# Optimization experiments

Measured on AMD Instinct MI355X. Metric: run time of the kernel, lower is better.

Reference implementation:

```python
import jax, jax.numpy as jnp
import numpy as np

B, S, D = 8, 4096, 1024
MINR, MAXR = 0.9, 0.999


def setup_inputs() -> dict:
    key = jax.random.key(0)
    ks = jax.random.split(key, 10)

    def dense(k, fin, fout):
        # lecun_normal-style init for flax nn.Dense kernels
        return jax.random.normal(k, (fin, fout), jnp.float32) * (fin ** -0.5)

    x = jax.random.normal(ks[0], (B, S, D), jnp.float32)
    # RNN 'a' param: stable_init -> uniform in [min_rad, max_rad]
    a_fwd = jax.random.uniform(ks[1], (D,), jnp.float32, MINR, MAXR)
    # RGLRU 'a' param: recurrence_init
    u = jax.random.uniform(ks[2], (D,), jnp.float32)
    log_rad = 0.5 * jnp.log(u * (MAXR ** 2 - MINR ** 2) + MINR ** 2)
    a_param = jnp.log(jnp.exp(-log_rad) - 1.0)
    return {
        "x": x,
        "a_fwd": a_fwd,
        "Wf1": dense(ks[3], D, D), "bf1": jnp.zeros((D,), jnp.float32),
        "Wf2": dense(ks[4], D, D), "bf2": jnp.zeros((D,), jnp.float32),
        "Wbx": dense(ks[5], D, D), "bbx": jnp.zeros((D,), jnp.float32),
        "Wgx": dense(ks[6], D, D), "bgx": jnp.zeros((D,), jnp.float32),
        "Wga": dense(ks[7], D, D), "bga": jnp.zeros((D,), jnp.float32),
        "a_param": a_param,
        "Wb2": dense(ks[8], D, D), "bb2": jnp.zeros((D,), jnp.float32),
    }


def reference(x, a_fwd, Wf1, bf1, Wf2, bf2, Wbx, bbx, Wgx, bgx, Wga, bga,
              a_param, Wb2, bb2):
    b = x.shape[0]
    d = Wf1.shape[1]
    identity = x
    xg = jax.nn.gelu(x)  # flax nn.gelu default = tanh approximation

    # ---- forward branch: plain linear RNN  h = a*h + x_t ----
    u = xg @ Wf1 + bf1                       # [B,S,D]
    u_sf = jnp.swapaxes(u, 0, 1)             # [S,B,D]

    def step_f(h, ut):
        h = a_fwd * h + ut
        return h, h

    _, hf = jax.lax.scan(step_f, jnp.zeros((b, d), u.dtype), u_sf)
    out_f = jnp.swapaxes(hf, 0, 1) @ Wf2 + bf2

    # ---- backward branch: RG-LRU, reversed scan ----
    v = xg @ Wbx + bbx                       # [B,S,D]
    gate_x = jax.nn.sigmoid(v @ Wgx + bgx)
    gate_a = jax.nn.sigmoid(v @ Wga + bga)
    log_a = -8.0 * gate_a * jax.nn.softplus(a_param)
    a = jnp.exp(log_a)                       # [B,S,D]
    # h = a*h + sqrt(1 - a^2) * (gate_x * v)
    scaled_in = jnp.sqrt(1.0 - jnp.exp(2.0 * log_a)) * (gate_x * v)

    a_sf = jnp.swapaxes(a, 0, 1)             # [S,B,D]
    in_sf = jnp.swapaxes(scaled_in, 0, 1)    # [S,B,D]

    def step_b(h, inp):
        a_t, g_t = inp
        h = a_t * h + g_t
        return h, h

    _, hb = jax.lax.scan(step_b, jnp.zeros((b, d), v.dtype), (a_sf, in_sf),
                         reverse=True)
    out_b = jnp.swapaxes(hb, 0, 1) @ Wb2 + bb2

    return out_f + out_b + identity
```

## Files before the change

### kernel.cpp

```cpp
#include <hip/hip_runtime.h>

typedef __bf16 bf16;
typedef __bf16 bf16x8 __attribute__((ext_vector_type(8)));
typedef float floatx4 __attribute__((ext_vector_type(4)));

typedef __attribute__((address_space(1))) const void gvoid_t;
typedef __attribute__((address_space(3))) void lvoid_t;

#define B_DIM 8
#define S_DIM 4096
#define M_DIM 32768
#define CHUNK 128
#define NCHUNK 32

__device__ __forceinline__ void gload_lds16(const bf16* g, bf16* l) {
    __builtin_amdgcn_global_load_lds((gvoid_t*)g, (lvoid_t*)l, 16, 0, 0);
}

__device__ __forceinline__ float gelu_tanh(float x) {
    float x3 = x * x * x;
    return 0.5f * x * (1.0f + tanhf(0.7978845608028654f * (x + 0.044715f * x3)));
}

__device__ __forceinline__ float sigmoidf(float z) {
    return 1.0f / (1.0f + expf(-z));
}

__global__ void prep_weights(const float* __restrict__ W0, const float* __restrict__ W1,
                             const float* __restrict__ W2, const float* __restrict__ W3,
                             const float* __restrict__ W4, const float* __restrict__ W5,
                             bf16* __restrict__ T0, bf16* __restrict__ T1,
                             bf16* __restrict__ T2, bf16* __restrict__ T3,
                             bf16* __restrict__ T4, bf16* __restrict__ T5) {
    __shared__ float tile[32][33];
    int mz = blockIdx.z;
    const float* W = mz == 0 ? W0 : mz == 1 ? W1 : mz == 2 ? W2 : mz == 3 ? W3 : mz == 4 ? W4 : W5;
    bf16* T = mz == 0 ? T0 : mz == 1 ? T1 : mz == 2 ? T2 : mz == 3 ? T3 : mz == 4 ? T4 : T5;
    int tn = blockIdx.x * 32;
    int tk = blockIdx.y * 32;
    int tx = threadIdx.x & 31, ty = threadIdx.x >> 5;
#pragma unroll
    for (int i = 0; i < 4; ++i)
        tile[ty + i * 8][tx] = W[(size_t)(tk + ty + i * 8) * 1024 + tn + tx];
    __syncthreads();
#pragma unroll
    for (int i = 0; i < 4; ++i)
        T[(size_t)(tn + ty + i * 8) * 1024 + tk + tx] = (bf16)tile[tx][ty + i * 8];
}

__global__ void sp_kernel(const float* __restrict__ a_param, float* __restrict__ spbuf) {
    int d = blockIdx.x * 256 + threadIdx.x;
    spbuf[d] = log1pf(expf(a_param[d]));
}

__global__ void gelu_kernel(const float* __restrict__ x, bf16* __restrict__ xg) {
    size_t i = (size_t)blockIdx.x * 256 + threadIdx.x;
    float4 v = ((const float4*)x)[i];
    bf16 o0 = (bf16)gelu_tanh(v.x), o1 = (bf16)gelu_tanh(v.y);
    bf16 o2 = (bf16)gelu_tanh(v.z), o3 = (bf16)gelu_tanh(v.w);
    typedef __bf16 bf16x4 __attribute__((ext_vector_type(4)));
    bf16x4 o = {o0, o1, o2, o3};
    ((bf16x4*)xg)[i] = o;
}

template <int MODE>
__launch_bounds__(256, 2)
__global__ void gemm_k1024(const bf16* __restrict__ A, const bf16* __restrict__ Bt,
                           float* __restrict__ outf, bf16* __restrict__ outh,
                           const float* __restrict__ bias,
                           const float* __restrict__ auxf,
                           const bf16* __restrict__ labuf,
                           const bf16* __restrict__ vbuf,
                           const float* __restrict__ bias2) {
    __shared__ __align__(16) bf16 lsA[128 * 64];
    __shared__ __align__(16) bf16 lsB[128 * 64];
    const int tid = threadIdx.x;
    const int wave = tid >> 6;
    const int lane = tid & 63;
    const int lane15 = lane & 15;
    const int quad = lane >> 4;
    const int wm = wave & 1, wn = wave >> 1;
    const int blk = blockIdx.x;
    const int xcd = blk & 7;
    const int j = blk >> 3;
    const long m0 = (long)(xcd * 32 + (j >> 3)) * 128;
    const long n0 = (long)(j & 7) * 128;
    const int r_in = lane >> 3;
    const int cch = lane & 7;

    floatx4 acc[4][4] = {};

    for (int kt = 0; kt < 16; ++kt) {
        __syncthreads();
#pragma unroll
        for (int i = 0; i < 4; ++i) {
            int rr = (i * 4 + wave) * 8 + r_in;
            int g = cch ^ (rr & 7);
            gload_lds16(A + (size_t)(m0 + rr) * 1024 + kt * 64 + g * 8, &lsA[(i * 4 + wave) * 512]);
            gload_lds16(Bt + (size_t)(n0 + rr) * 1024 + kt * 64 + g * 8, &lsB[(i * 4 + wave) * 512]);
        }
        __syncthreads();
#pragma unroll
        for (int kk = 0; kk < 2; ++kk) {
            bf16x8 af[4], bfr[4];
#pragma unroll
            for (int mi = 0; mi < 4; ++mi) {
                int ml = wm * 64 + mi * 16 + lane15;
                af[mi] = *(const bf16x8*)&lsA[ml * 64 + ((kk * 4 + quad) ^ (ml & 7)) * 8];
            }
#pragma unroll
            for (int ni = 0; ni < 4; ++ni) {
                int nl = wn * 64 + ni * 16 + lane15;
                bfr[ni] = *(const bf16x8*)&lsB[nl * 64 + ((kk * 4 + quad) ^ (nl & 7)) * 8];
            }
#pragma unroll
            for (int mi = 0; mi < 4; ++mi)
#pragma unroll
                for (int ni = 0; ni < 4; ++ni)
                    acc[mi][ni] = __builtin_amdgcn_mfma_f32_16x16x32_bf16(af[mi], bfr[ni], acc[mi][ni], 0, 0, 0);
        }
    }

#pragma unroll
    for (int mi = 0; mi < 4; ++mi) {
#pragma unroll
        for (int ni = 0; ni < 4; ++ni) {
            floatx4 v = acc[mi][ni];
            long gn = n0 + wn * 64 + ni * 16 + lane15;
#pragma unroll
            for (int r = 0; r < 4; ++r) {
                long gm = m0 + wm * 64 + mi * 16 + quad * 4 + r;
                size_t o = (size_t)gm * 1024 + gn;
                if (MODE == 0) {
                    outf[o] = v[r] + bias[gn];
                } else if (MODE == 1) {
                    outh[o] = (bf16)(v[r] + bias[gn]);
                } else if (MODE == 2) {
                    float z = v[r] + bias[gn];
                    outh[o] = (bf16)(-8.0f * sigmoidf(z) * auxf[gn]);
                } else if (MODE == 3) {
                    float z = v[r] + bias[gn];
                    float laf = (float)labuf[o];
                    float sc = sqrtf(-expm1f(2.0f * laf)) * sigmoidf(z) * (float)vbuf[o];
                    outh[o] = (bf16)sc;
                } else if (MODE == 4) {
                    outf[o] = v[r] + bias[gn] + bias2[gn] + auxf[o];
                } else {
                    outf[o] += v[r];
                }
            }
        }
    }
}

__global__ void fscan1(const float* __restrict__ u, const float* __restrict__ a_fwd,
                       float* __restrict__ carry) {
    int d = (blockIdx.x & 3) * 256 + threadIdx.x;
    int c = (blockIdx.x >> 2) & 31;
    int b = blockIdx.x >> 7;
    float a = a_fwd[d];
    const float* up = u + ((size_t)(b * S_DIM + c * CHUNK)) * 1024 + d;
    float h = 0.0f;
#pragma unroll 8
    for (int t = 0; t < CHUNK; ++t) h = fmaf(a, h, up[(size_t)t * 1024]);
    carry[((size_t)c * 8 + b) * 1024 + d] = h;
}
__global__ void fscan2(const float* __restrict__ carry, const float* __restrict__ a_fwd,
                       float* __restrict__ H) {
    int idx = blockIdx.x * 256 + threadIdx.x;
    int d = idx & 1023, b = idx >> 10;
    float a = a_fwd[d];
    float aL = a;
#pragma unroll
    for (int i = 0; i < 7; ++i) aL *= aL;
    float h = 0.0f;
    for (int c = 0; c < NCHUNK; ++c) {
        size_t o = ((size_t)c * 8 + b) * 1024 + d;
        H[o] = h;
        h = fmaf(aL, h, carry[o]);
    }
}
__global__ void fscan3(const float* __restrict__ u, const float* __restrict__ a_fwd,
                       const float* __restrict__ H, bf16* __restrict__ hf) {
    int d = (blockIdx.x & 3) * 256 + threadIdx.x;
    int c = (blockIdx.x >> 2) & 31;
    int b = blockIdx.x >> 7;
    float a = a_fwd[d];
    const float* up = u + ((size_t)(b * S_DIM + c * CHUNK)) * 1024 + d;
    bf16* op = hf + ((size_t)(b * S_DIM + c * CHUNK)) * 1024 + d;
    float h = H[((size_t)c * 8 + b) * 1024 + d];
#pragma unroll 4
    for (int t = 0; t < CHUNK; ++t) {
        h = fmaf(a, h, up[(size_t)t * 1024]);
        op[(size_t)t * 1024] = (bf16)h;
    }
}

__global__ void bscan1(const bf16* __restrict__ la, const bf16* __restrict__ sc,
                       float* __restrict__ BL, float* __restrict__ BP) {
    int d = (blockIdx.x & 3) * 256 + threadIdx.x;
    int c = (blockIdx.x >> 2) & 31;
    int b = blockIdx.x >> 7;
    const bf16* lap = la + ((size_t)(b * S_DIM + c * CHUNK)) * 1024 + d;
    const bf16* gp = sc + ((size_t)(b * S_DIM + c * CHUNK)) * 1024 + d;
    float h = 0.0f, slog = 0.0f;
#pragma unroll 4
    for (int t = CHUNK - 1; t >= 0; --t) {
        float laf = (float)lap[(size_t)t * 1024];
        h = fmaf(expf(laf), h, (float)gp[(size_t)t * 1024]);
        slog += laf;
    }
    size_t o = ((size_t)c * 8 + b) * 1024 + d;
    BL[o] = h;
    BP[o] = expf(slog);
}
__global__ void bscan2(const float* __restrict__ BL, const float* __restrict__ BP,
                       float* __restrict__ R) {
    int idx = blockIdx.x * 256 + threadIdx.x;
    int d = idx & 1023, b = idx >> 10;
    float r = 0.0f;
    for (int c = NCHUNK - 1; c >= 0; --c) {
        size_t o = ((size_t)c * 8 + b) * 1024 + d;
        R[o] = r;
        r = fmaf(BP[o], r, BL[o]);
    }
}
__global__ void bscan3(const bf16* __restrict__ la, const bf16* __restrict__ sc,
                       const float* __restrict__ R, bf16* __restrict__ hb) {
    int d = (blockIdx.x & 3) * 256 + threadIdx.x;
    int c = (blockIdx.x >> 2) & 31;
    int b = blockIdx.x >> 7;
    const bf16* lap = la + ((size_t)(b * S_DIM + c * CHUNK)) * 1024 + d;
    const bf16* gp = sc + ((size_t)(b * S_DIM + c * CHUNK)) * 1024 + d;
    bf16* op = hb + ((size_t)(b * S_DIM + c * CHUNK)) * 1024 + d;
    float h = R[((size_t)c * 8 + b) * 1024 + d];
#pragma unroll 4
    for (int t = CHUNK - 1; t >= 0; --t) {
        h = fmaf(expf((float)lap[(size_t)t * 1024]), h, (float)gp[(size_t)t * 1024]);
        op[(size_t)t * 1024] = (bf16)h;
    }
}

extern "C" void kernel_launch(void* const* d_in, const int* in_sizes, int n_in,
                              void* d_out, int out_size, void* d_ws, size_t ws_size,
                              hipStream_t stream) {
    const float* x       = (const float*)d_in[0];
    const float* a_fwd   = (const float*)d_in[1];
    const float* Wf1     = (const float*)d_in[2];
    const float* bf1     = (const float*)d_in[3];
    const float* Wf2     = (const float*)d_in[4];
    const float* bf2     = (const float*)d_in[5];
    const float* Wbx     = (const float*)d_in[6];
    const float* bbx     = (const float*)d_in[7];
    const float* Wgx     = (const float*)d_in[8];
    const float* bgx     = (const float*)d_in[9];
    const float* Wga     = (const float*)d_in[10];
    const float* bga     = (const float*)d_in[11];
    const float* a_param = (const float*)d_in[12];
    const float* Wb2     = (const float*)d_in[13];
    const float* bb2     = (const float*)d_in[14];
    float* out = (float*)d_out;
    (void)in_sizes; (void)n_in; (void)out_size; (void)ws_size;

    char* ws = (char*)d_ws;
    size_t off = 0;
    const size_t WSZ = (size_t)1024 * 1024 * 2;
    bf16* Wf1t = (bf16*)(ws + off); off += WSZ;
    bf16* Wbxt = (bf16*)(ws + off); off += WSZ;
    bf16* Wgxt = (bf16*)(ws + off); off += WSZ;
    bf16* Wgat = (bf16*)(ws + off); off += WSZ;
    bf16* Wf2t = (bf16*)(ws + off); off += WSZ;
    bf16* Wb2t = (bf16*)(ws + off); off += WSZ;
    float* spbuf = (float*)(ws + off); off += 4096;
    const size_t BSZ = (size_t)M_DIM * 1024 * 2;
    bf16* buf0 = (bf16*)(ws + off); off += BSZ;
    bf16* buf1 = (bf16*)(ws + off); off += BSZ;
    bf16* buf2 = (bf16*)(ws + off); off += BSZ;
    float* Fc = (float*)(ws + off); off += (size_t)NCHUNK * 8 * 1024 * 4;
    float* FH = (float*)(ws + off); off += (size_t)NCHUNK * 8 * 1024 * 4;
    float* BL = (float*)(ws + off); off += (size_t)NCHUNK * 8 * 1024 * 4;
    float* BP = (float*)(ws + off); off += (size_t)NCHUNK * 8 * 1024 * 4;
    float* BR = (float*)(ws + off); off += (size_t)NCHUNK * 8 * 1024 * 4;

    bf16* xg = buf0;
    bf16* hf = buf0;
    bf16* vb = buf1;
    bf16* hb = buf1;
    bf16* la = buf2;
    float* u = (float*)d_out;
    bf16* sc = (bf16*)d_out;

    prep_weights<<<dim3(32, 32, 6), 256, 0, stream>>>(Wf1, Wbx, Wgx, Wga, Wf2, Wb2,
                                                      Wf1t, Wbxt, Wgxt, Wgat, Wf2t, Wb2t);
    sp_kernel<<<4, 256, 0, stream>>>(a_param, spbuf);
    gelu_kernel<<<32768, 256, 0, stream>>>(x, xg);
    gemm_k1024<0><<<2048, 256, 0, stream>>>(xg, Wf1t, u, nullptr, bf1, nullptr, nullptr, nullptr, nullptr);
    gemm_k1024<1><<<2048, 256, 0, stream>>>(xg, Wbxt, nullptr, vb, bbx, nullptr, nullptr, nullptr, nullptr);
    fscan1<<<1024, 256, 0, stream>>>(u, a_fwd, Fc);
    fscan2<<<32, 256, 0, stream>>>(Fc, a_fwd, FH);
    fscan3<<<1024, 256, 0, stream>>>(u, a_fwd, FH, hf);
    gemm_k1024<2><<<2048, 256, 0, stream>>>(vb, Wgat, nullptr, la, bga, spbuf, nullptr, nullptr, nullptr);
    gemm_k1024<3><<<2048, 256, 0, stream>>>(vb, Wgxt, nullptr, sc, bgx, nullptr, la, vb, nullptr);
    bscan1<<<1024, 256, 0, stream>>>(la, sc, BL, BP);
    bscan2<<<32, 256, 0, stream>>>(BL, BP, BR);
    bscan3<<<1024, 256, 0, stream>>>(la, sc, BR, hb);
    gemm_k1024<4><<<2048, 256, 0, stream>>>(hf, Wf2t, out, nullptr, bf2, x, nullptr, nullptr, bb2);
    gemm_k1024<5><<<2048, 256, 0, stream>>>(hb, Wb2t, out, nullptr, nullptr, nullptr, nullptr, nullptr, nullptr);
}
```

Before: 967.4 us.

## Fuse paired GEMMs sharing an A operand and concatenate the final output GEMMs along K

The two GEMMs that read xg, and the two gate GEMMs that read v, now each run as one dual-output kernel that loads the A tile once and accumulates against two B tiles. The two output projections become a single K=2048 GEMM over a concatenated weight, with residual and both biases folded in, so the read-modify-write of out goes away. The forward pre-activation u is stored as bf16 instead of fp32, and the scan kernels process four channels per thread with vector loads and stores. In exchange the dual kernel carries twice the accumulator registers and more LDS, which may lower occupancy, and u loses precision.

```diff
diff --git a/kernel.cpp b/kernel.cpp
--- a/kernel.cpp
+++ b/kernel.cpp
@@ -2,6 +2,7 @@
 
 typedef __bf16 bf16;
 typedef __bf16 bf16x8 __attribute__((ext_vector_type(8)));
+typedef __bf16 bf16x4 __attribute__((ext_vector_type(4)));
 typedef float floatx4 __attribute__((ext_vector_type(4)));
 
 typedef __attribute__((address_space(1))) const void gvoid_t;
@@ -31,11 +32,10 @@
                              const float* __restrict__ W4, const float* __restrict__ W5,
                              bf16* __restrict__ T0, bf16* __restrict__ T1,
                              bf16* __restrict__ T2, bf16* __restrict__ T3,
-                             bf16* __restrict__ T4, bf16* __restrict__ T5) {
+                             bf16* __restrict__ Bcat) {
     __shared__ float tile[32][33];
     int mz = blockIdx.z;
     const float* W = mz == 0 ? W0 : mz == 1 ? W1 : mz == 2 ? W2 : mz == 3 ? W3 : mz == 4 ? W4 : W5;
-    bf16* T = mz == 0 ? T0 : mz == 1 ? T1 : mz == 2 ? T2 : mz == 3 ? T3 : mz == 4 ? T4 : T5;
     int tn = blockIdx.x * 32;
     int tk = blockIdx.y * 32;
     int tx = threadIdx.x & 31, ty = threadIdx.x >> 5;
@@ -43,9 +43,17 @@
     for (int i = 0; i < 4; ++i)
         tile[ty + i * 8][tx] = W[(size_t)(tk + ty + i * 8) * 1024 + tn + tx];
     __syncthreads();
-#pragma unroll
-    for (int i = 0; i < 4; ++i)
-        T[(size_t)(tn + ty + i * 8) * 1024 + tk + tx] = (bf16)tile[tx][ty + i * 8];
+    if (mz < 4) {
+        bf16* T = mz == 0 ? T0 : mz == 1 ? T1 : mz == 2 ? T2 : T3;
+#pragma unroll
+        for (int i = 0; i < 4; ++i)
+            T[(size_t)(tn + ty + i * 8) * 1024 + tk + tx] = (bf16)tile[tx][ty + i * 8];
+    } else {
+        int koff = (mz == 5) ? 1024 : 0;
+#pragma unroll
+        for (int i = 0; i < 4; ++i)
+            Bcat[(size_t)(tn + ty + i * 8) * 2048 + koff + tk + tx] = (bf16)tile[tx][ty + i * 8];
+    }
 }
 
 __global__ void sp_kernel(const float* __restrict__ a_param, float* __restrict__ spbuf) {
@@ -56,22 +64,109 @@
 __global__ void gelu_kernel(const float* __restrict__ x, bf16* __restrict__ xg) {
     size_t i = (size_t)blockIdx.x * 256 + threadIdx.x;
     float4 v = ((const float4*)x)[i];
-    bf16 o0 = (bf16)gelu_tanh(v.x), o1 = (bf16)gelu_tanh(v.y);
-    bf16 o2 = (bf16)gelu_tanh(v.z), o3 = (bf16)gelu_tanh(v.w);
-    typedef __bf16 bf16x4 __attribute__((ext_vector_type(4)));
-    bf16x4 o = {o0, o1, o2, o3};
+    bf16x4 o;
+    o[0] = (bf16)gelu_tanh(v.x); o[1] = (bf16)gelu_tanh(v.y);
+    o[2] = (bf16)gelu_tanh(v.z); o[3] = (bf16)gelu_tanh(v.w);
     ((bf16x4*)xg)[i] = o;
 }
 
 template <int MODE>
 __launch_bounds__(256, 2)
-__global__ void gemm_k1024(const bf16* __restrict__ A, const bf16* __restrict__ Bt,
-                           float* __restrict__ outf, bf16* __restrict__ outh,
-                           const float* __restrict__ bias,
-                           const float* __restrict__ auxf,
-                           const bf16* __restrict__ labuf,
-                           const bf16* __restrict__ vbuf,
-                           const float* __restrict__ bias2) {
+__global__ void gemm_dual(const bf16* __restrict__ A, const bf16* __restrict__ B1t,
+                          const bf16* __restrict__ B2t,
+                          bf16* __restrict__ out1, bf16* __restrict__ out2,
+                          const float* __restrict__ bias1, const float* __restrict__ bias2,
+                          const float* __restrict__ spbuf, const bf16* __restrict__ vbuf) {
+    __shared__ __align__(16) bf16 lsA[128 * 64];
+    __shared__ __align__(16) bf16 lsB1[128 * 64];
+    __shared__ __align__(16) bf16 lsB2[128 * 64];
+    const int tid = threadIdx.x;
+    const int wave = tid >> 6;
+    const int lane = tid & 63;
+    const int lane15 = lane & 15;
+    const int quad = lane >> 4;
+    const int wm = wave & 1, wn = wave >> 1;
+    const int blk = blockIdx.x;
+    const int xcd = blk & 7;
+    const int j = blk >> 3;
+    const long m0 = (long)(xcd * 32 + (j >> 3)) * 128;
+    const long n0 = (long)(j & 7) * 128;
+    const int r_in = lane >> 3;
+    const int cch = lane & 7;
+
+    floatx4 acc1[4][4] = {};
+    floatx4 acc2[4][4] = {};
+
+    for (int kt = 0; kt < 16; ++kt) {
+        __syncthreads();
+#pragma unroll
+        for (int i = 0; i < 4; ++i) {
+            int rr = (i * 4 + wave) * 8 + r_in;
+            int g = cch ^ (rr & 7);
+            gload_lds16(A + (size_t)(m0 + rr) * 1024 + kt * 64 + g * 8, &lsA[(i * 4 + wave) * 512]);
+            gload_lds16(B1t + (size_t)(n0 + rr) * 1024 + kt * 64 + g * 8, &lsB1[(i * 4 + wave) * 512]);
+            gload_lds16(B2t + (size_t)(n0 + rr) * 1024 + kt * 64 + g * 8, &lsB2[(i * 4 + wave) * 512]);
+        }
+        __syncthreads();
+#pragma unroll
+        for (int kk = 0; kk < 2; ++kk) {
+            bf16x8 af[4], b1f[4], b2f[4];
+#pragma unroll
+            for (int mi = 0; mi < 4; ++mi) {
+                int ml = wm * 64 + mi * 16 + lane15;
+                af[mi] = *(const bf16x8*)&lsA[ml * 64 + ((kk * 4 + quad) ^ (ml & 7)) * 8];
+            }
+#pragma unroll
+            for (int ni = 0; ni < 4; ++ni) {
+                int nl = wn * 64 + ni * 16 + lane15;
+                int idx = nl * 64 + ((kk * 4 + quad) ^ (nl & 7)) * 8;
+                b1f[ni] = *(const bf16x8*)&lsB1[idx];
+                b2f[ni] = *(const bf16x8*)&lsB2[idx];
+            }
+#pragma unroll
+            for (int mi = 0; mi < 4; ++mi)
+#pragma unroll
+                for (int ni = 0; ni < 4; ++ni) {
+                    acc1[mi][ni] = __builtin_amdgcn_mfma_f32_16x16x32_bf16(af[mi], b1f[ni], acc1[mi][ni], 0, 0, 0);
+                    acc2[mi][ni] = __builtin_amdgcn_mfma_f32_16x16x32_bf16(af[mi], b2f[ni], acc2[mi][ni], 0, 0, 0);
+                }
+        }
+    }
+
+#pragma unroll
+    for (int mi = 0; mi < 4; ++mi) {
+#pragma unroll
+        for (int ni = 0; ni < 4; ++ni) {
+            floatx4 v1 = acc1[mi][ni];
+            floatx4 v2 = acc2[mi][ni];
+            long gn = n0 + wn * 64 + ni * 16 + lane15;
+            float bb1 = bias1[gn], bb2 = bias2[gn];
+            float sp = (MODE == 1) ? spbuf[gn] : 0.0f;
+#pragma unroll
+            for (int r = 0; r < 4; ++r) {
+                long gm = m0 + wm * 64 + mi * 16 + quad * 4 + r;
+                size_t o = (size_t)gm * 1024 + gn;
+                if (MODE == 0) {
+                    out1[o] = (bf16)(v1[r] + bb1);
+                    out2[o] = (bf16)(v2[r] + bb2);
+                } else {
+                    float za = v2[r] + bb2;
+                    float la = -8.0f * sigmoidf(za) * sp;
+                    out2[o] = (bf16)la;
+                    float zx = v1[r] + bb1;
+                    float sc = sqrtf(-expm1f(2.0f * la)) * sigmoidf(zx) * (float)vbuf[o];
+                    out1[o] = (bf16)sc;
+                }
+            }
+        }
+    }
+}
+
+__launch_bounds__(256, 2)
+__global__ void gemm_fin(const bf16* __restrict__ A1, const bf16* __restrict__ A2,
+                         const bf16* __restrict__ Bcat, float* __restrict__ out,
+                         const float* __restrict__ bias1, const float* __restrict__ bias2,
+                         const float* __restrict__ xres) {
     __shared__ __align__(16) bf16 lsA[128 * 64];
     __shared__ __align__(16) bf16 lsB[128 * 64];
     const int tid = threadIdx.x;
@@ -90,14 +185,16 @@
 
     floatx4 acc[4][4] = {};
 
-    for (int kt = 0; kt < 16; ++kt) {
+    for (int kt = 0; kt < 32; ++kt) {
+        const bf16* Asrc = (kt < 16) ? A1 : A2;
+        int ktt = kt & 15;
         __syncthreads();
 #pragma unroll
         for (int i = 0; i < 4; ++i) {
             int rr = (i * 4 + wave) * 8 + r_in;
             int g = cch ^ (rr & 7);
-            gload_lds16(A + (size_t)(m0 + rr) * 1024 + kt * 64 + g * 8, &lsA[(i * 4 + wave) * 512]);
-            gload_lds16(Bt + (size_t)(n0 + rr) * 1024 + kt * 64 + g * 8, &lsB[(i * 4 + wave) * 512]);
+            gload_lds16(Asrc + (size_t)(m0 + rr) * 1024 + ktt * 64 + g * 8, &lsA[(i * 4 + wave) * 512]);
+            gload_lds16(Bcat + (size_t)(n0 + rr) * 2048 + kt * 64 + g * 8, &lsB[(i * 4 + wave) * 512]);
         }
         __syncthreads();
 #pragma unroll
@@ -127,43 +224,34 @@
         for (int ni = 0; ni < 4; ++ni) {
             floatx4 v = acc[mi][ni];
             long gn = n0 + wn * 64 + ni * 16 + lane15;
+            float bb = bias1[gn] + bias2[gn];
 #pragma unroll
             for (int r = 0; r < 4; ++r) {
                 long gm = m0 + wm * 64 + mi * 16 + quad * 4 + r;
                 size_t o = (size_t)gm * 1024 + gn;
-                if (MODE == 0) {
-                    outf[o] = v[r] + bias[gn];
-                } else if (MODE == 1) {
-                    outh[o] = (bf16)(v[r] + bias[gn]);
-                } else if (MODE == 2) {
-                    float z = v[r] + bias[gn];
-                    outh[o] = (bf16)(-8.0f * sigmoidf(z) * auxf[gn]);
-                } else if (MODE == 3) {
-                    float z = v[r] + bias[gn];
-                    float laf = (float)labuf[o];
-                    float sc = sqrtf(-expm1f(2.0f * laf)) * sigmoidf(z) * (float)vbuf[o];
-                    outh[o] = (bf16)sc;
-                } else if (MODE == 4) {
-                    outf[o] = v[r] + bias[gn] + bias2[gn] + auxf[o];
-                } else {
-                    outf[o] += v[r];
-                }
-            }
-        }
-    }
-}
-
-__global__ void fscan1(const float* __restrict__ u, const float* __restrict__ a_fwd,
+                out[o] = v[r] + bb + xres[o];
+            }
+        }
+    }
+}
+
+__global__ void fscan1(const bf16* __restrict__ u, const float* __restrict__ a_fwd,
                        float* __restrict__ carry) {
-    int d = (blockIdx.x & 3) * 256 + threadIdx.x;
-    int c = (blockIdx.x >> 2) & 31;
-    int b = blockIdx.x >> 7;
-    float a = a_fwd[d];
-    const float* up = u + ((size_t)(b * S_DIM + c * CHUNK)) * 1024 + d;
-    float h = 0.0f;
-#pragma unroll 8
-    for (int t = 0; t < CHUNK; ++t) h = fmaf(a, h, up[(size_t)t * 1024]);
-    carry[((size_t)c * 8 + b) * 1024 + d] = h;
+    int b = blockIdx.x >> 5, c = blockIdx.x & 31;
+    int d0 = threadIdx.x * 4;
+    float4 a4 = *(const float4*)(a_fwd + d0);
+    const bf16* up = u + ((size_t)(b * S_DIM + c * CHUNK)) * 1024 + d0;
+    float h0 = 0, h1 = 0, h2 = 0, h3 = 0;
+#pragma unroll 4
+    for (int t = 0; t < CHUNK; ++t) {
+        bf16x4 uv = *(const bf16x4*)(up + (size_t)t * 1024);
+        h0 = fmaf(a4.x, h0, (float)uv[0]);
+        h1 = fmaf(a4.y, h1, (float)uv[1]);
+        h2 = fmaf(a4.z, h2, (float)uv[2]);
+        h3 = fmaf(a4.w, h3, (float)uv[3]);
+    }
+    float4 st = {h0, h1, h2, h3};
+    *(float4*)(carry + ((size_t)c * 8 + b) * 1024 + d0) = st;
 }
 __global__ void fscan2(const float* __restrict__ carry, const float* __restrict__ a_fwd,
                        float* __restrict__ H) {
@@ -180,39 +268,49 @@
         h = fmaf(aL, h, carry[o]);
     }
 }
-__global__ void fscan3(const float* __restrict__ u, const float* __restrict__ a_fwd,
+__global__ void fscan3(const bf16* __restrict__ u, const float* __restrict__ a_fwd,
                        const float* __restrict__ H, bf16* __restrict__ hf) {
-    int d = (blockIdx.x & 3) * 256 + threadIdx.x;
-    int c = (blockIdx.x >> 2) & 31;
-    int b = blockIdx.x >> 7;
-    float a = a_fwd[d];
-    const float* up = u + ((size_t)(b * S_DIM + c * CHUNK)) * 1024 + d;
-    bf16* op = hf + ((size_t)(b * S_DIM + c * CHUNK)) * 1024 + d;
-    float h = H[((size_t)c * 8 + b) * 1024 + d];
+    int b = blockIdx.x >> 5, c = blockIdx.x & 31;
+    int d0 = threadIdx.x * 4;
+    float4 a4 = *(const float4*)(a_fwd + d0);
+    const bf16* up = u + ((size_t)(b * S_DIM + c * CHUNK)) * 1024 + d0;
+    bf16* op = hf + ((size_t)(b * S_DIM + c * CHUNK)) * 1024 + d0;
+    float4 h = *(const float4*)(H + ((size_t)c * 8 + b) * 1024 + d0);
 #pragma unroll 4
     for (int t = 0; t < CHUNK; ++t) {
-        h = fmaf(a, h, up[(size_t)t * 1024]);
-        op[(size_t)t * 1024] = (bf16)h;
+        bf16x4 uv = *(const bf16x4*)(up + (size_t)t * 1024);
+        h.x = fmaf(a4.x, h.x, (float)uv[0]);
+        h.y = fmaf(a4.y, h.y, (float)uv[1]);
+        h.z = fmaf(a4.z, h.z, (float)uv[2]);
+        h.w = fmaf(a4.w, h.w, (float)uv[3]);
+        bf16x4 o = {(bf16)h.x, (bf16)h.y, (bf16)h.z, (bf16)h.w};
+        *(bf16x4*)(op + (size_t)t * 1024) = o;
     }
 }
 
 __global__ void bscan1(const bf16* __restrict__ la, const bf16* __restrict__ sc,
                        float* __restrict__ BL, float* __restrict__ BP) {
-    int d = (blockIdx.x & 3) * 256 + threadIdx.x;
-    int c = (blockIdx.x >> 2) & 31;
-    int b = blockIdx.x >> 7;
-    const bf16* lap = la + ((size_t)(b * S_DIM + c * CHUNK)) * 1024 + d;
-    const bf16* gp = sc + ((size_t)(b * S_DIM + c * CHUNK)) * 1024 + d;
-    float h = 0.0f, slog = 0.0f;
+    int b = blockIdx.x >> 5, c = blockIdx.x & 31;
+    int d0 = threadIdx.x * 4;
+    const bf16* lap = la + ((size_t)(b * S_DIM + c * CHUNK)) * 1024 + d0;
+    const bf16* gp = sc + ((size_t)(b * S_DIM + c * CHUNK)) * 1024 + d0;
+    float h0 = 0, h1 = 0, h2 = 0, h3 = 0;
+    float s0 = 0, s1 = 0, s2 = 0, s3 = 0;
 #pragma unroll 4
     for (int t = CHUNK - 1; t >= 0; --t) {
-        float laf = (float)lap[(size_t)t * 1024];
-        h = fmaf(expf(laf), h, (float)gp[(size_t)t * 1024]);
-        slog += laf;
-    }
-    size_t o = ((size_t)c * 8 + b) * 1024 + d;
-    BL[o] = h;
-    BP[o] = expf(slog);
+        bf16x4 lv = *(const bf16x4*)(lap + (size_t)t * 1024);
+        bf16x4 gv = *(const bf16x4*)(gp + (size_t)t * 1024);
+        float l0 = (float)lv[0], l1 = (float)lv[1], l2 = (float)lv[2], l3 = (float)lv[3];
+        h0 = fmaf(expf(l0), h0, (float)gv[0]); s0 += l0;
+        h1 = fmaf(expf(l1), h1, (float)gv[1]); s1 += l1;
+        h2 = fmaf(expf(l2), h2, (float)gv[2]); s2 += l2;
+        h3 = fmaf(expf(l3), h3, (float)gv[3]); s3 += l3;
+    }
+    size_t o = ((size_t)c * 8 + b) * 1024 + d0;
+    float4 hl = {h0, h1, h2, h3};
+    float4 pp = {expf(s0), expf(s1), expf(s2), expf(s3)};
+    *(float4*)(BL + o) = hl;
+    *(float4*)(BP + o) = pp;
 }
 __global__ void bscan2(const float* __restrict__ BL, const float* __restrict__ BP,
                        float* __restrict__ R) {
@@ -227,17 +325,22 @@
 }
 __global__ void bscan3(const bf16* __restrict__ la, const bf16* __restrict__ sc,
                        const float* __restrict__ R, bf16* __restrict__ hb) {
-    int d = (blockIdx.x & 3) * 256 + threadIdx.x;
-    int c = (blockIdx.x >> 2) & 31;
-    int b = blockIdx.x >> 7;
-    const bf16* lap = la + ((size_t)(b * S_DIM + c * CHUNK)) * 1024 + d;
-    const bf16* gp = sc + ((size_t)(b * S_DIM + c * CHUNK)) * 1024 + d;
-    bf16* op = hb + ((size_t)(b * S_DIM + c * CHUNK)) * 1024 + d;
-    float h = R[((size_t)c * 8 + b) * 1024 + d];
+    int b = blockIdx.x >> 5, c = blockIdx.x & 31;
+    int d0 = threadIdx.x * 4;
+    const bf16* lap = la + ((size_t)(b * S_DIM + c * CHUNK)) * 1024 + d0;
+    const bf16* gp = sc + ((size_t)(b * S_DIM + c * CHUNK)) * 1024 + d0;
+    bf16* op = hb + ((size_t)(b * S_DIM + c * CHUNK)) * 1024 + d0;
+    float4 h = *(const float4*)(R + ((size_t)c * 8 + b) * 1024 + d0);
 #pragma unroll 4
     for (int t = CHUNK - 1; t >= 0; --t) {
-        h = fmaf(expf((float)lap[(size_t)t * 1024]), h, (float)gp[(size_t)t * 1024]);
-        op[(size_t)t * 1024] = (bf16)h;
+        bf16x4 lv = *(const bf16x4*)(lap + (size_t)t * 1024);
+        bf16x4 gv = *(const bf16x4*)(gp + (size_t)t * 1024);
+        h.x = fmaf(expf((float)lv[0]), h.x, (float)gv[0]);
+        h.y = fmaf(expf((float)lv[1]), h.y, (float)gv[1]);
+        h.z = fmaf(expf((float)lv[2]), h.z, (float)gv[2]);
+        h.w = fmaf(expf((float)lv[3]), h.w, (float)gv[3]);
+        bf16x4 o = {(bf16)h.x, (bf16)h.y, (bf16)h.z, (bf16)h.w};
+        *(bf16x4*)(op + (size_t)t * 1024) = o;
     }
 }
 
@@ -269,8 +372,7 @@
     bf16* Wbxt = (bf16*)(ws + off); off += WSZ;
     bf16* Wgxt = (bf16*)(ws + off); off += WSZ;
     bf16* Wgat = (bf16*)(ws + off); off += WSZ;
-    bf16* Wf2t = (bf16*)(ws + off); off += WSZ;
-    bf16* Wb2t = (bf16*)(ws + off); off += WSZ;
+    bf16* Bcat = (bf16*)(ws + off); off += 2 * WSZ;
     float* spbuf = (float*)(ws + off); off += 4096;
     const size_t BSZ = (size_t)M_DIM * 1024 * 2;
     bf16* buf0 = (bf16*)(ws + off); off += BSZ;
@@ -287,23 +389,20 @@
     bf16* vb = buf1;
     bf16* hb = buf1;
     bf16* la = buf2;
-    float* u = (float*)d_out;
-    bf16* sc = (bf16*)d_out;
+    bf16* u  = (bf16*)d_out;
+    bf16* sc = (bf16*)d_out + (size_t)M_DIM * 1024;
 
     prep_weights<<<dim3(32, 32, 6), 256, 0, stream>>>(Wf1, Wbx, Wgx, Wga, Wf2, Wb2,
-                                                      Wf1t, Wbxt, Wgxt, Wgat, Wf2t, Wb2t);
+                                                      Wf1t, Wbxt, Wgxt, Wgat, Bcat);
     sp_kernel<<<4, 256, 0, stream>>>(a_param, spbuf);
     gelu_kernel<<<32768, 256, 0, stream>>>(x, xg);
-    gemm_k1024<0><<<2048, 256, 0, stream>>>(xg, Wf1t, u, nullptr, bf1, nullptr, nullptr, nullptr, nullptr);
-    gemm_k1024<1><<<2048, 256, 0, stream>>>(xg, Wbxt, nullptr, vb, bbx, nullptr, nullptr, nullptr, nullptr);
-    fscan1<<<1024, 256, 0, stream>>>(u, a_fwd, Fc);
+    gemm_dual<0><<<2048, 256, 0, stream>>>(xg, Wf1t, Wbxt, u, vb, bf1, bbx, nullptr, nullptr);
+    fscan1<<<256, 256, 0, stream>>>(u, a_fwd, Fc);
     fscan2<<<32, 256, 0, stream>>>(Fc, a_fwd, FH);
-    fscan3<<<1024, 256, 0, stream>>>(u, a_fwd, FH, hf);
-    gemm_k1024<2><<<2048, 256, 0, stream>>>(vb, Wgat, nullptr, la, bga, spbuf, nullptr, nullptr, nullptr);
-    gemm_k1024<3><<<2048, 256, 0, stream>>>(vb, Wgxt, nullptr, sc, bgx, nullptr, la, vb, nullptr);
-    bscan1<<<1024, 256, 0, stream>>>(la, sc, BL, BP);
+    fscan3<<<256, 256, 0, stream>>>(u, a_fwd, FH, hf);
+    gemm_dual<1><<<2048, 256, 0, stream>>>(vb, Wgxt, Wgat, sc, la, bgx, bga, spbuf, vb);
+    bscan1<<<256, 256, 0, stream>>>(la, sc, BL, BP);
     bscan2<<<32, 256, 0, stream>>>(BL, BP, BR);
-    bscan3<<<1024, 256, 0, stream>>>(la, sc, BR, hb);
-    gemm_k1024<4><<<2048, 256, 0, stream>>>(hf, Wf2t, out, nullptr, bf2, x, nullptr, nullptr, bb2);
-    gemm_k1024<5><<<2048, 256, 0, stream>>>(hb, Wb2t, out, nullptr, nullptr, nullptr, nullptr, nullptr, nullptr);
-}
+    bscan3<<<256, 256, 0, stream>>>(la, sc, BR, hb);
+    gemm_fin<<<2048, 256, 0, stream>>>(hf, hb, Bcat, out, bf2, bb2, x);
+}
```

Result: slower. 988.5 us (+2.2%).
